# Optimization experiments

Hardware: AMD Instinct MI355X
Metric: run time of the kernel (lower is better)

The kernel has to match this reference:

```python
import jax, jax.numpy as jnp
import numpy as np

B, NIN, L, N, K, NOUT = 4096, 512, 16, 512, 32, 256
TOTAL = NIN + L * N  # 8704 total nodes in the DAG


def setup_inputs() -> dict:
    key = jax.random.key(0)
    ks = jax.random.split(key, 5)
    x = jax.random.normal(ks[0], (B, NIN), jnp.float32)
    W = jax.random.normal(ks[1], (L, N, K), jnp.float32) * 0.2
    b = jax.random.normal(ks[2], (L, N), jnp.float32) * 0.1
    W_out = jax.random.normal(ks[3], (NOUT, K), jnp.float32) * 0.2
    b_out = jax.random.normal(ks[4], (NOUT,), jnp.float32) * 0.1
    rng = np.random.default_rng(0)
    # layer l may only read nodes computed before it (topological validity)
    idx = np.stack([rng.integers(0, NIN + l * N, size=(N, K)) for l in range(L)]).astype(np.int32)
    idx_out = rng.integers(0, TOTAL, size=(NOUT, K)).astype(np.int32)
    return {"x": x, "W": W, "b": b, "W_out": W_out, "b_out": b_out,
            "idx": jnp.asarray(idx), "idx_out": jnp.asarray(idx_out)}


def reference(x, W, b, W_out, b_out, idx, idx_out):
    # buffer of all node activations, filled topologically (out_dict analog)
    buf0 = jnp.zeros((B, TOTAL), x.dtype).at[:, :NIN].set(x)

    def step(carry, layer):
        buf, l = carry
        li, lW, lb = layer
        gathered = buf[:, li]  # [B, N, K] irregular gather of predecessor outputs
        out = jax.nn.sigmoid(jnp.einsum('bnk,nk->bn', gathered, lW) + lb)  # per-node tiny linear + sigmoid
        buf = jax.lax.dynamic_update_slice(buf, out, (0, NIN + l * N))
        return (buf, l + 1), None

    (buf, _), _ = jax.lax.scan(step, (buf0, jnp.int32(0)), (idx, W, b))
    g = buf[:, idx_out]  # [B, NOUT, K]
    return jax.nn.sigmoid(jnp.einsum('bok,ok->bo', g, W_out) + b_out)
```

## Files before the change

kernel.cpp:

```cpp
#include <hip/hip_runtime.h>
#include <hip/hip_fp16.h>
#include <math.h>

#define B     4096
#define NIN   512
#define L     16
#define N     512
#define K     32
#define NOUT  256
#define TOTAL (NIN + L * N)
#define BROWS 4
#define BLOCK 512

typedef __attribute__((ext_vector_type(4))) _Float16 h4;
typedef __attribute__((ext_vector_type(8))) _Float16 h8;
typedef __attribute__((ext_vector_type(8))) unsigned short u16x8;

__device__ __forceinline__ float sigmoidf_fast(float z) {
    return 1.0f / (1.0f + __expf(-z));
}

__global__ void repack_kernel(const float* __restrict__ W,
                              const int*   __restrict__ idx,
                              const float* __restrict__ W_out,
                              const int*   __restrict__ idx_out,
                              _Float16* __restrict__ wh,
                              unsigned short* __restrict__ i16,
                              _Float16* __restrict__ who,
                              unsigned short* __restrict__ io16)
{
    int g = blockIdx.x * 256 + threadIdx.x;
    if (g < L * N * K) {
        wh[g]  = (_Float16)W[g];
        i16[g] = (unsigned short)idx[g];
    } else {
        int h = g - L * N * K;
        if (h < NOUT * K) {
            who[h]  = (_Float16)W_out[h];
            io16[h] = (unsigned short)idx_out[h];
        }
    }
}

__global__ __launch_bounds__(BLOCK, 4)
void ffnet_kernel(const float* __restrict__ x,
                  const float* __restrict__ b,
                  const float* __restrict__ b_out,
                  const _Float16*       __restrict__ wh,
                  const unsigned short* __restrict__ i16,
                  const _Float16*       __restrict__ who,
                  const unsigned short* __restrict__ io16,
                  float* __restrict__ out)
{
    __shared__ h4 buf[TOTAL];

    const int t  = threadIdx.x;
    const int r0 = blockIdx.x * BROWS;

    {
        h4 v;
        v.x = (_Float16)x[(size_t)(r0 + 0) * NIN + t];
        v.y = (_Float16)x[(size_t)(r0 + 1) * NIN + t];
        v.z = (_Float16)x[(size_t)(r0 + 2) * NIN + t];
        v.w = (_Float16)x[(size_t)(r0 + 3) * NIN + t];
        buf[t] = v;
    }

    u16x8 ni[4];
    {
        const u16x8* ip = (const u16x8*)(i16 + (size_t)t * K);
        ni[0] = ip[0]; ni[1] = ip[1]; ni[2] = ip[2]; ni[3] = ip[3];
    }
    __syncthreads();

#define GATHER8(CI, W8)                                                        \
    {                                                                          \
        _Pragma("unroll")                                                      \
        for (int j = 0; j < 8; ++j) {                                          \
            const int   c = (int)(CI)[j];                                      \
            const float w = (float)(W8)[j];                                    \
            const h4    v = buf[c];                                            \
            acc.x = fmaf((float)v.x, w, acc.x);                                \
            acc.y = fmaf((float)v.y, w, acc.y);                                \
            acc.z = fmaf((float)v.z, w, acc.z);                                \
            acc.w = fmaf((float)v.w, w, acc.w);                                \
        }                                                                      \
    }

    for (int l = 0; l < L; ++l) {
        u16x8 ci[4];
        ci[0] = ni[0]; ci[1] = ni[1]; ci[2] = ni[2]; ci[3] = ni[3];

        const h8* wp = (const h8*)(wh + ((size_t)l * N + t) * K);
        const h8 w0 = wp[0], w1 = wp[1], w2 = wp[2], w3 = wp[3];

        if (l + 1 < L) {
            const u16x8* np = (const u16x8*)(i16 + ((size_t)(l + 1) * N + t) * K);
            ni[0] = np[0]; ni[1] = np[1]; ni[2] = np[2]; ni[3] = np[3];
        }

        float4 acc = make_float4(0.f, 0.f, 0.f, 0.f);
        GATHER8(ci[0], w0)
        GATHER8(ci[1], w1)
        GATHER8(ci[2], w2)
        GATHER8(ci[3], w3)

        const float bb = b[l * N + t];
        h4 o;
        o.x = (_Float16)sigmoidf_fast(acc.x + bb);
        o.y = (_Float16)sigmoidf_fast(acc.y + bb);
        o.z = (_Float16)sigmoidf_fast(acc.z + bb);
        o.w = (_Float16)sigmoidf_fast(acc.w + bb);
        buf[NIN + l * N + t] = o;
        __syncthreads();
    }

    if (t < NOUT) {
        const u16x8* ip = (const u16x8*)(io16 + (size_t)t * K);
        const h8*    wp = (const h8*)   (who  + (size_t)t * K);
        const u16x8 i0 = ip[0], i1 = ip[1], i2 = ip[2], i3 = ip[3];
        const h8    w0 = wp[0], w1 = wp[1], w2 = wp[2], w3 = wp[3];

        float4 acc = make_float4(0.f, 0.f, 0.f, 0.f);
        GATHER8(i0, w0)
        GATHER8(i1, w1)
        GATHER8(i2, w2)
        GATHER8(i3, w3)

        const float bb = b_out[t];
        out[(size_t)(r0 + 0) * NOUT + t] = sigmoidf_fast(acc.x + bb);
        out[(size_t)(r0 + 1) * NOUT + t] = sigmoidf_fast(acc.y + bb);
        out[(size_t)(r0 + 2) * NOUT + t] = sigmoidf_fast(acc.z + bb);
        out[(size_t)(r0 + 3) * NOUT + t] = sigmoidf_fast(acc.w + bb);
    }
#undef GATHER8
}

extern "C" void kernel_launch(void* const* d_in, const int* in_sizes, int n_in,
                              void* d_out, int out_size, void* d_ws, size_t ws_size,
                              hipStream_t stream) {
    const float* x     = (const float*)d_in[0];
    const float* W     = (const float*)d_in[1];
    const float* b     = (const float*)d_in[2];
    const float* W_out = (const float*)d_in[3];
    const float* b_out = (const float*)d_in[4];
    const int*   idx   = (const int*)d_in[5];
    const int*   idx_o = (const int*)d_in[6];
    float* out = (float*)d_out;

    char* ws = (char*)d_ws;
    _Float16*       wh   = (_Float16*)      (ws);
    unsigned short* i16  = (unsigned short*)(ws + 524288);
    _Float16*       who  = (_Float16*)      (ws + 1048576);
    unsigned short* io16 = (unsigned short*)(ws + 1048576 + 16384);

    const int total_pack = L * N * K + NOUT * K;
    repack_kernel<<<dim3((total_pack + 255) / 256), dim3(256), 0, stream>>>(
        W, idx, W_out, idx_o, wh, i16, who, io16);

    ffnet_kernel<<<dim3(B / BROWS), dim3(BLOCK), 0, stream>>>(
        x, b, b_out, wh, i16, who, io16, out);
}
```

Baseline: 160.1 us.

## Pack 8 batch rows per block with u8 activations and half2 FMAs

Intermediate activations are stored as 8-bit quantized values (round(a*256)) in shared memory, so 8 batch rows fit per block instead of 4. Inputs stay fp16 in a separate table. Accumulation moves to packed half2 FMAs, and u8 values are converted to fp16 with a byte-permute magic-number trick. The repack kernel sorts each node's predecessors (x first), pre-scales weights by 1/256, and folds the 0.5 dequant offset into the bias. This halves per-row shared traffic and doubles FMA throughput, at the cost of much lower precision: u8 activations and fp16 accumulation over 32 terms could break tolerance.

New measurement: 206.3 us. 28.9% more time.

```diff
diff --git a/kernel.cpp b/kernel.cpp
--- a/kernel.cpp
+++ b/kernel.cpp
@@ -9,61 +9,99 @@
 #define K     32
 #define NOUT  256
 #define TOTAL (NIN + L * N)
-#define BROWS 4
+#define NACT  (L * N)
+#define BROWS 8
 #define BLOCK 512
-
-typedef __attribute__((ext_vector_type(4))) _Float16 h4;
-typedef __attribute__((ext_vector_type(8))) _Float16 h8;
+#define NROWS (L * N + NOUT)
+
 typedef __attribute__((ext_vector_type(8))) unsigned short u16x8;
 
 __device__ __forceinline__ float sigmoidf_fast(float z) {
     return 1.0f / (1.0f + __expf(-z));
 }
+__device__ __forceinline__ __half2 bch2(unsigned int u) {
+    return __builtin_bit_cast(__half2, u);
+}
+__device__ __forceinline__ unsigned int h2u(float a, float b) {
+    unsigned short lo = __builtin_bit_cast(unsigned short, __float2half(a));
+    unsigned short hi = __builtin_bit_cast(unsigned short, __float2half(b));
+    return ((unsigned int)hi << 16) | lo;
+}
 
 __global__ void repack_kernel(const float* __restrict__ W,
                               const int*   __restrict__ idx,
+                              const float* __restrict__ b,
                               const float* __restrict__ W_out,
+                              const float* __restrict__ b_out,
                               const int*   __restrict__ idx_out,
-                              _Float16* __restrict__ wh,
+                              unsigned int*   __restrict__ wh2,
                               unsigned short* __restrict__ i16,
-                              _Float16* __restrict__ who,
-                              unsigned short* __restrict__ io16)
+                              float* __restrict__ bq,
+                              float* __restrict__ bqo)
 {
-    int g = blockIdx.x * 256 + threadIdx.x;
-    if (g < L * N * K) {
-        wh[g]  = (_Float16)W[g];
-        i16[g] = (unsigned short)idx[g];
-    } else {
-        int h = g - L * N * K;
-        if (h < NOUT * K) {
-            who[h]  = (_Float16)W_out[h];
-            io16[h] = (unsigned short)idx_out[h];
-        }
+    __shared__ int   tc[256];
+    __shared__ float tw[256];
+    const int t = threadIdx.x;
+    const int r = blockIdx.x * 8 + (t >> 5);
+    const int k = t & 31;
+
+    const bool is_out = (r >= L * N);
+    const int  ro     = r - L * N;
+    const float w = is_out ? W_out[(size_t)ro * K + k] : W[(size_t)r * K + k];
+    const int   c = is_out ? idx_out[(size_t)ro * K + k] : idx[(size_t)r * K + k];
+
+    const int lane = threadIdx.x & 63;
+    const unsigned long long bal = __ballot(c < NIN);
+    const unsigned gm = (unsigned)(bal >> (lane & 32));
+    const unsigned lowmask = (1u << (lane & 31)) - 1u;
+    const int nx = __popc(gm);
+    const int before_x = __popc(gm & lowmask);
+    const int pos = (c < NIN) ? before_x : (nx + ((lane & 31) - before_x));
+    const int base = t & ~31;
+    tc[base + pos] = c;
+    tw[base + pos] = w;
+    __syncthreads();
+    const int   sc = tc[t];
+    const float sw = tw[t];
+
+    const float weff = (sc < NIN) ? sw : sw * (1.0f / 256.0f);
+    wh2[(size_t)r * K + k] = h2u(weff, weff);
+    i16[(size_t)r * K + k] = (unsigned short)sc;
+
+    float s = (sc >= NIN) ? 0.5f * sw : 0.0f;
+    #pragma unroll
+    for (int off = 1; off < 32; off <<= 1) s += __shfl_xor(s, off, 32);
+    if (k == 0) {
+        if (is_out) bqo[ro] = b_out[ro] + s;
+        else        bq[r]   = b[r] + s;
     }
 }
 
 __global__ __launch_bounds__(BLOCK, 4)
 void ffnet_kernel(const float* __restrict__ x,
-                  const float* __restrict__ b,
-                  const float* __restrict__ b_out,
-                  const _Float16*       __restrict__ wh,
+                  const unsigned int*   __restrict__ wh2,
                   const unsigned short* __restrict__ i16,
-                  const _Float16*       __restrict__ who,
-                  const unsigned short* __restrict__ io16,
+                  const float* __restrict__ bq,
+                  const float* __restrict__ bqo,
                   float* __restrict__ out)
 {
-    __shared__ h4 buf[TOTAL];
+    __shared__ uint2 act[NACT];
+    __shared__ uint4 xh[NIN];
 
     const int t  = threadIdx.x;
     const int r0 = blockIdx.x * BROWS;
 
     {
-        h4 v;
-        v.x = (_Float16)x[(size_t)(r0 + 0) * NIN + t];
-        v.y = (_Float16)x[(size_t)(r0 + 1) * NIN + t];
-        v.z = (_Float16)x[(size_t)(r0 + 2) * NIN + t];
-        v.w = (_Float16)x[(size_t)(r0 + 3) * NIN + t];
-        buf[t] = v;
+        float xv[8];
+        #pragma unroll
+        for (int rr = 0; rr < 8; ++rr)
+            xv[rr] = x[(size_t)(r0 + rr) * NIN + t];
+        uint4 v;
+        v.x = h2u(xv[0], xv[1]);
+        v.y = h2u(xv[2], xv[3]);
+        v.z = h2u(xv[4], xv[5]);
+        v.w = h2u(xv[6], xv[7]);
+        xh[t] = v;
     }
 
     u16x8 ni[4];
@@ -73,67 +111,103 @@
     }
     __syncthreads();
 
-#define GATHER8(CI, W8)                                                        \
-    {                                                                          \
-        _Pragma("unroll")                                                      \
-        for (int j = 0; j < 8; ++j) {                                          \
-            const int   c = (int)(CI)[j];                                      \
-            const float w = (float)(W8)[j];                                    \
-            const h4    v = buf[c];                                            \
-            acc.x = fmaf((float)v.x, w, acc.x);                                \
-            acc.y = fmaf((float)v.y, w, acc.y);                                \
-            acc.z = fmaf((float)v.z, w, acc.z);                                \
-            acc.w = fmaf((float)v.w, w, acc.w);                                \
-        }                                                                      \
+#define GATHER1(C, W2)                                                          \
+    {                                                                           \
+        const int c_ = (C);                                                     \
+        const __half2 w2_ = (W2);                                               \
+        if (c_ < NIN) {                                                         \
+            const uint4 v_ = xh[c_];                                            \
+            a0 = __hfma2(bch2(v_.x), w2_, a0);                                  \
+            a1 = __hfma2(bch2(v_.y), w2_, a1);                                  \
+            a2 = __hfma2(bch2(v_.z), w2_, a2);                                  \
+            a3 = __hfma2(bch2(v_.w), w2_, a3);                                  \
+        } else {                                                                \
+            const uint2 q_ = act[c_ - NIN];                                     \
+            const unsigned d0_ = __builtin_amdgcn_perm(0x64646464u, q_.x, 0x05010400u); \
+            const unsigned d1_ = __builtin_amdgcn_perm(0x64646464u, q_.x, 0x05030402u); \
+            const unsigned d2_ = __builtin_amdgcn_perm(0x64646464u, q_.y, 0x05010400u); \
+            const unsigned d3_ = __builtin_amdgcn_perm(0x64646464u, q_.y, 0x05030402u); \
+            const __half2 bias_ = bch2(0x64806480u);   \
+            a0 = __hfma2(__hsub2(bch2(d0_), bias_), w2_, a0);                   \
+            a1 = __hfma2(__hsub2(bch2(d1_), bias_), w2_, a1);                   \
+            a2 = __hfma2(__hsub2(bch2(d2_), bias_), w2_, a2);                   \
+            a3 = __hfma2(__hsub2(bch2(d3_), bias_), w2_, a3);                   \
+        }                                                                       \
     }
 
     for (int l = 0; l < L; ++l) {
-        u16x8 ci[4];
-        ci[0] = ni[0]; ci[1] = ni[1]; ci[2] = ni[2]; ci[3] = ni[3];
-
-        const h8* wp = (const h8*)(wh + ((size_t)l * N + t) * K);
-        const h8 w0 = wp[0], w1 = wp[1], w2 = wp[2], w3 = wp[3];
+        u16x8 ci[4] = { ni[0], ni[1], ni[2], ni[3] };
+
+        unsigned wu[32];
+        {
+            const uint4* wp = (const uint4*)(wh2 + ((size_t)l * N + t) * K);
+            #pragma unroll
+            for (int g = 0; g < 8; ++g) {
+                const uint4 w4 = wp[g];
+                wu[4*g] = w4.x; wu[4*g+1] = w4.y; wu[4*g+2] = w4.z; wu[4*g+3] = w4.w;
+            }
+        }
+        const float bb = bq[l * N + t];
 
         if (l + 1 < L) {
             const u16x8* np = (const u16x8*)(i16 + ((size_t)(l + 1) * N + t) * K);
             ni[0] = np[0]; ni[1] = np[1]; ni[2] = np[2]; ni[3] = np[3];
         }
 
-        float4 acc = make_float4(0.f, 0.f, 0.f, 0.f);
-        GATHER8(ci[0], w0)
-        GATHER8(ci[1], w1)
-        GATHER8(ci[2], w2)
-        GATHER8(ci[3], w3)
-
-        const float bb = b[l * N + t];
-        h4 o;
-        o.x = (_Float16)sigmoidf_fast(acc.x + bb);
-        o.y = (_Float16)sigmoidf_fast(acc.y + bb);
-        o.z = (_Float16)sigmoidf_fast(acc.z + bb);
-        o.w = (_Float16)sigmoidf_fast(acc.w + bb);
-        buf[NIN + l * N + t] = o;
+        __half2 a0 = bch2(0u), a1 = bch2(0u), a2 = bch2(0u), a3 = bch2(0u);
+        #pragma unroll
+        for (int g = 0; g < 4; ++g) {
+            #pragma unroll
+            for (int j = 0; j < 8; ++j)
+                GATHER1((int)ci[g][j], bch2(wu[g * 8 + j]));
+        }
+
+        const float zf[8] = {
+            __low2float(a0), __high2float(a0), __low2float(a1), __high2float(a1),
+            __low2float(a2), __high2float(a2), __low2float(a3), __high2float(a3)
+        };
+        unsigned u8[8];
+        #pragma unroll
+        for (int rr = 0; rr < 8; ++rr) {
+            const float a = sigmoidf_fast(zf[rr] + bb);
+            u8[rr] = (unsigned)fminf(rintf(a * 256.0f), 255.0f);
+        }
+        uint2 pk;
+        pk.x = u8[0] | (u8[1] << 8) | (u8[2] << 16) | (u8[3] << 24);
+        pk.y = u8[4] | (u8[5] << 8) | (u8[6] << 16) | (u8[7] << 24);
+        act[l * N + t] = pk;
         __syncthreads();
     }
 
     if (t < NOUT) {
-        const u16x8* ip = (const u16x8*)(io16 + (size_t)t * K);
-        const h8*    wp = (const h8*)   (who  + (size_t)t * K);
-        const u16x8 i0 = ip[0], i1 = ip[1], i2 = ip[2], i3 = ip[3];
-        const h8    w0 = wp[0], w1 = wp[1], w2 = wp[2], w3 = wp[3];
-
-        float4 acc = make_float4(0.f, 0.f, 0.f, 0.f);
-        GATHER8(i0, w0)
-        GATHER8(i1, w1)
-        GATHER8(i2, w2)
-        GATHER8(i3, w3)
-
-        const float bb = b_out[t];
-        out[(size_t)(r0 + 0) * NOUT + t] = sigmoidf_fast(acc.x + bb);
-        out[(size_t)(r0 + 1) * NOUT + t] = sigmoidf_fast(acc.y + bb);
-        out[(size_t)(r0 + 2) * NOUT + t] = sigmoidf_fast(acc.z + bb);
-        out[(size_t)(r0 + 3) * NOUT + t] = sigmoidf_fast(acc.w + bb);
-    }
-#undef GATHER8
+        const u16x8* ip = (const u16x8*)(i16 + ((size_t)(L * N) + t) * K);
+        u16x8 oi[4] = { ip[0], ip[1], ip[2], ip[3] };
+        unsigned wu[32];
+        {
+            const uint4* wp = (const uint4*)(wh2 + ((size_t)(L * N) + t) * K);
+            #pragma unroll
+            for (int g = 0; g < 8; ++g) {
+                const uint4 w4 = wp[g];
+                wu[4*g] = w4.x; wu[4*g+1] = w4.y; wu[4*g+2] = w4.z; wu[4*g+3] = w4.w;
+            }
+        }
+        __half2 a0 = bch2(0u), a1 = bch2(0u), a2 = bch2(0u), a3 = bch2(0u);
+        #pragma unroll
+        for (int g = 0; g < 4; ++g) {
+            #pragma unroll
+            for (int j = 0; j < 8; ++j)
+                GATHER1((int)oi[g][j], bch2(wu[g * 8 + j]));
+        }
+        const float bb = bqo[t];
+        const float zf[8] = {
+            __low2float(a0), __high2float(a0), __low2float(a1), __high2float(a1),
+            __low2float(a2), __high2float(a2), __low2float(a3), __high2float(a3)
+        };
+        #pragma unroll
+        for (int rr = 0; rr < 8; ++rr)
+            out[(size_t)(r0 + rr) * NOUT + t] = sigmoidf_fast(zf[rr] + bb);
+    }
+#undef GATHER1
 }
 
 extern "C" void kernel_launch(void* const* d_in, const int* in_sizes, int n_in,
@@ -149,15 +223,14 @@
     float* out = (float*)d_out;
 
     char* ws = (char*)d_ws;
-    _Float16*       wh   = (_Float16*)      (ws);
-    unsigned short* i16  = (unsigned short*)(ws + 524288);
-    _Float16*       who  = (_Float16*)      (ws + 1048576);
-    unsigned short* io16 = (unsigned short*)(ws + 1048576 + 16384);
-
-    const int total_pack = L * N * K + NOUT * K;
-    repack_kernel<<<dim3((total_pack + 255) / 256), dim3(256), 0, stream>>>(
-        W, idx, W_out, idx_o, wh, i16, who, io16);
+    unsigned int*   wh2  = (unsigned int*)  (ws);
+    unsigned short* i16  = (unsigned short*)(ws + 1081344);
+    float*          bq   = (float*)         (ws + 1081344 + 540672);
+    float*          bqo  = (float*)         (ws + 1081344 + 540672 + 32768);
+
+    repack_kernel<<<dim3(NROWS / 8), dim3(256), 0, stream>>>(
+        W, idx, b, W_out, b_out, idx_o, wh2, i16, bq, bqo);
 
     ffnet_kernel<<<dim3(B / BROWS), dim3(BLOCK), 0, stream>>>(
-        x, b, b_out, wh, i16, who, io16, out);
-}
+        x, wh2, i16, bq, bqo, out);
+}
```
